# Optimization experiments

Measured on AMD Instinct MI355X. Metric: run time of the kernel, lower is better.

## Reference

```python
import jax, jax.numpy as jnp
import numpy as np

NUM_HEADS = 16
ROTARY_BASE = 10000.0


def _apply_rotary(x):
    # x: (B, S, H, D); GPT-NeoX style rotate-half over full head dim
    B, S, H, D = x.shape
    half = D // 2
    inv_freq = 1.0 / (ROTARY_BASE ** (jnp.arange(0, half, dtype=jnp.float32) / half))
    t = jnp.arange(S, dtype=jnp.float32)
    freqs = jnp.einsum('s,d->sd', t, inv_freq)          # (S, half)
    cos = jnp.cos(freqs)[None, :, None, :]               # (1, S, 1, half)
    sin = jnp.sin(freqs)[None, :, None, :]
    x1, x2 = x[..., :half], x[..., half:]
    return jnp.concatenate([x1 * cos - x2 * sin, x2 * cos + x1 * sin], axis=-1).astype(x.dtype)


def setup_inputs() -> dict:
    key = jax.random.key(0)
    k0, k1, k2 = jax.random.split(key, 3)
    B, S, E = 2, 2048, 2048
    x = jax.random.normal(k0, (B, S, E), dtype=jnp.float32)
    wqkv = jax.random.normal(k1, (3 * E, E), dtype=jnp.float32) * 0.02
    bqkv = jnp.zeros((3 * E,), dtype=jnp.float32)
    wout = jax.random.normal(k2, (E, E), dtype=jnp.float32) * 0.02
    bout = jnp.zeros((E,), dtype=jnp.float32)
    return {"x": x, "wqkv": wqkv, "bqkv": bqkv, "wout": wout, "bout": bout}


def reference(x, wqkv, bqkv, wout, bout):
    B, S, E = x.shape
    H = NUM_HEADS
    D = E // H
    # fused QKV projection: (B, S, 3, H, D)
    qkv = (jnp.einsum('bse,fe->bsf', x, wqkv) + bqkv).reshape(B, S, 3, H, D)
    q, k, v = qkv[:, :, 0], qkv[:, :, 1], qkv[:, :, 2]
    q = _apply_rotary(q)
    k = _apply_rotary(k)
    scale = 1.0 / jnp.sqrt(jnp.float32(D))
    scores = jnp.einsum('bthd,bshd->bhts', q, k) * scale  # (B, H, S, S)
    causal_mask = jnp.triu(jnp.full((S, S), -10000.0, dtype=scores.dtype), 1)
    attn = jax.nn.softmax(scores + causal_mask, axis=-1)
    ctx = jnp.einsum('bhts,bshd->bthd', attn, v).reshape(B, S, E)
    return jnp.einsum('bse,fe->bsf', ctx, wout) + bout
```

## Files before the change

kernel.cpp:

```cpp
#include <hip/hip_runtime.h>
#include <math.h>

#define BB 2
#define SS 2048
#define EE 2048
#define HH 16
#define DD 128
#define FF 6144

typedef __attribute__((ext_vector_type(8))) short short8;
typedef __attribute__((ext_vector_type(4))) float floatx4;

static __device__ __forceinline__ unsigned short f2bf(float x) {
  unsigned u = __float_as_uint(x);
  u += 0x7fffu + ((u >> 16) & 1u);
  return (unsigned short)(u >> 16);
}
static __device__ __forceinline__ float bf2f(unsigned short h) {
  return __uint_as_float((unsigned)h << 16);
}

#define GLOAD_LDS16(gp, lp)                                       \
  __builtin_amdgcn_global_load_lds(                               \
      (const __attribute__((address_space(1))) void*)(gp),        \
      (__attribute__((address_space(3))) void*)(lp), 16, 0, 0)

__global__ __launch_bounds__(256) void cast_f32_bf16(
    const float* __restrict__ in, unsigned short* __restrict__ out, int n4) {
  const int i = blockIdx.x * 256 + threadIdx.x;
  if (i >= n4) return;
  const float4 v = ((const float4*)in)[i];
  ushort4 o;
  o.x = f2bf(v.x); o.y = f2bf(v.y); o.z = f2bf(v.z); o.w = f2bf(v.w);
  ((ushort4*)out)[i] = o;
}

static __device__ __forceinline__ void store_out(float* p, float v) { *p = v; }
static __device__ __forceinline__ void store_out(unsigned short* p, float v) {
  *p = f2bf(v);
}

template <typename OutT>
__global__ __launch_bounds__(256) void gemm_bf16_mfma(
    const unsigned short* __restrict__ A, const unsigned short* __restrict__ Bt,
    const float* __restrict__ bias, OutT* __restrict__ C,
    int M, int N, int K) {
  __shared__ unsigned short As[2][128][32];
  __shared__ unsigned short Bs[2][128][32];
  const int tid = threadIdx.x;
  const int L = tid & 63;
  const int w = tid >> 6;
  const int m0 = blockIdx.y * 128;
  const int n0 = blockIdx.x * 128;

  const int i0 = w * 2;
  const int lrow = L >> 2;
  const int lcol = (L & 3) * 8;
  const size_t a_off0 = (size_t)(m0 + (i0 + 0) * 16 + lrow) * K + lcol;
  const size_t a_off1 = (size_t)(m0 + (i0 + 1) * 16 + lrow) * K + lcol;
  const size_t b_off0 = (size_t)(n0 + (i0 + 0) * 16 + lrow) * K + lcol;
  const size_t b_off1 = (size_t)(n0 + (i0 + 1) * 16 + lrow) * K + lcol;

  const int wr = (w >> 1) * 64;
  const int wc = (w & 1) * 64;
  const int lane16 = L & 15;
  const int quad = L >> 4;

  floatx4 acc[4][4] = {};

  GLOAD_LDS16(A + a_off0, &As[0][(i0 + 0) * 16][0]);
  GLOAD_LDS16(A + a_off1, &As[0][(i0 + 1) * 16][0]);
  GLOAD_LDS16(Bt + b_off0, &Bs[0][(i0 + 0) * 16][0]);
  GLOAD_LDS16(Bt + b_off1, &Bs[0][(i0 + 1) * 16][0]);

  for (int k0 = 0; k0 < K; k0 += 32) {
    const int cur = (k0 >> 5) & 1;
    __syncthreads();
    if (k0 + 32 < K) {
      const int nxt = cur ^ 1;
      GLOAD_LDS16(A + a_off0 + k0 + 32, &As[nxt][(i0 + 0) * 16][0]);
      GLOAD_LDS16(A + a_off1 + k0 + 32, &As[nxt][(i0 + 1) * 16][0]);
      GLOAD_LDS16(Bt + b_off0 + k0 + 32, &Bs[nxt][(i0 + 0) * 16][0]);
      GLOAD_LDS16(Bt + b_off1 + k0 + 32, &Bs[nxt][(i0 + 1) * 16][0]);
    }

    short8 a[4], b[4];
#pragma unroll
    for (int mi = 0; mi < 4; ++mi)
      a[mi] = *(const short8*)(&As[cur][wr + mi * 16 + lane16][quad * 8]);
#pragma unroll
    for (int ni = 0; ni < 4; ++ni)
      b[ni] = *(const short8*)(&Bs[cur][wc + ni * 16 + lane16][quad * 8]);
#pragma unroll
    for (int mi = 0; mi < 4; ++mi)
#pragma unroll
      for (int ni = 0; ni < 4; ++ni)
        acc[mi][ni] = __builtin_amdgcn_mfma_f32_16x16x32_bf16(
            a[mi], b[ni], acc[mi][ni], 0, 0, 0);
  }

#pragma unroll
  for (int ni = 0; ni < 4; ++ni) {
    const int col = n0 + wc + ni * 16 + lane16;
    const float bv = bias[col];
#pragma unroll
    for (int mi = 0; mi < 4; ++mi) {
      const int row = m0 + wr + mi * 16 + quad * 4;
#pragma unroll
      for (int r = 0; r < 4; ++r)
        store_out(&C[(size_t)(row + r) * N + col], acc[mi][ni][r] + bv);
    }
  }
}

template <typename OutT>
__global__ __launch_bounds__(512, 2) void gemm256_8ph(
    const unsigned short* __restrict__ A, const unsigned short* __restrict__ Bt,
    const float* __restrict__ bias, OutT* __restrict__ C,
    int M, int N, int K) {
  __shared__ __align__(16) unsigned short As[2][16384];
  __shared__ __align__(16) unsigned short Bs[2][16384];

  const int tid = threadIdx.x;
  const int w = tid >> 6;
  const int L = tid & 63;
  const int lane16 = L & 15;
  const int quad = L >> 4;
  const int wm = w >> 2;
  const int wn = w & 3;

  const int nby = M >> 8;
  const int q8 = gridDim.x >> 3;
  const int wg = (blockIdx.x & 7) * q8 + (blockIdx.x >> 3);
  const int by = wg % nby;
  const int bx = wg / nby;
  const int m0 = by << 8;
  const int n0 = bx << 8;

  const int lA = ((w >> 1) << 4) + (L >> 2);
  const int scol = ((w & 1) << 5) + (((L & 3) * 8) ^ ((L & 32) ? 16 : 0));
  unsigned aoff[4], boff[4];
#pragma unroll
  for (int j = 0; j < 4; ++j) {
    const int ra = ((j & 1) << 7) | ((j >> 1) << 6) | lA;
    aoff[j] = (unsigned)(m0 + ra) * (unsigned)K + scol;
    const int lB = j * 64 + lA;
    const int rB = (((lB >> 5) & 3) << 6) | (((lB >> 7) & 1) << 5) | (lB & 31);
    boff[j] = (unsigned)(n0 + rB) * (unsigned)K + scol;
  }
  const int ldst = w * 512;

  const int sq = (quad * 8) ^ ((lane16 & 8) << 1);
  const int rbase = lane16 * 32 + sq;

  floatx4 acc[8][4] = {};

  GLOAD_LDS16(A + aoff[0], &As[0][0 * 4096 + ldst]);
  GLOAD_LDS16(A + aoff[1], &As[0][1 * 4096 + ldst]);
  GLOAD_LDS16(Bt + boff[0], &Bs[0][0 * 4096 + ldst]);
  GLOAD_LDS16(Bt + boff[1], &Bs[0][1 * 4096 + ldst]);
  GLOAD_LDS16(Bt + boff[2], &Bs[0][2 * 4096 + ldst]);
  GLOAD_LDS16(Bt + boff[3], &Bs[0][3 * 4096 + ldst]);
  GLOAD_LDS16(A + aoff[2], &As[0][2 * 4096 + ldst]);
  GLOAD_LDS16(A + aoff[3], &As[0][3 * 4096 + ldst]);
  GLOAD_LDS16(A + aoff[0] + 64, &As[1][0 * 4096 + ldst]);
  GLOAD_LDS16(A + aoff[1] + 64, &As[1][1 * 4096 + ldst]);
  GLOAD_LDS16(Bt + boff[0] + 64, &Bs[1][0 * 4096 + ldst]);
  GLOAD_LDS16(Bt + boff[1] + 64, &Bs[1][1 * 4096 + ldst]);
  GLOAD_LDS16(Bt + boff[2] + 64, &Bs[1][2 * 4096 + ldst]);
  GLOAD_LDS16(Bt + boff[3] + 64, &Bs[1][3 * 4096 + ldst]);
  GLOAD_LDS16(A + aoff[2] + 64, &As[1][2 * 4096 + ldst]);
  GLOAD_LDS16(A + aoff[3] + 64, &As[1][3 * 4096 + ldst]);
  asm volatile("s_waitcnt vmcnt(8)" ::: "memory");
  __builtin_amdgcn_sched_barrier(0);
  __builtin_amdgcn_s_barrier();

  const int NT = K >> 6;
  short8 a[4][2], b0[2][2], b1[2][2];

  for (int t = 0; t < NT; ++t) {
    const int c = t & 1;
    const unsigned kn2 = (unsigned)(t + 2) << 6;
    const unsigned short* Ac = &As[c][0];
    const unsigned short* Bc = &Bs[c][0];

#pragma unroll
    for (int i = 0; i < 4; ++i)
#pragma unroll
      for (int kk = 0; kk < 2; ++kk)
        a[i][kk] = *(const short8*)(Ac + ((wm * 4 + i) * 2 + kk) * 512 + rbase);
#pragma unroll
    for (int j = 0; j < 2; ++j)
#pragma unroll
      for (int kk = 0; kk < 2; ++kk)
        b0[j][kk] = *(const short8*)(Bc + ((wn * 2 + j) * 2 + kk) * 512 + rbase);
    __builtin_amdgcn_s_setprio(1);
#pragma unroll
    for (int i = 0; i < 4; ++i)
#pragma unroll
      for (int j = 0; j < 2; ++j)
#pragma unroll
        for (int kk = 0; kk < 2; ++kk)
          acc[i][j] = __builtin_amdgcn_mfma_f32_16x16x32_bf16(
              a[i][kk], b0[j][kk], acc[i][j], 0, 0, 0);
    __builtin_amdgcn_s_setprio(0);
    __builtin_amdgcn_sched_barrier(0);
    __builtin_amdgcn_s_barrier();

#pragma unroll
    for (int j = 0; j < 2; ++j)
#pragma unroll
      for (int kk = 0; kk < 2; ++kk)
        b1[j][kk] =
            *(const short8*)(Bc + ((8 + wn * 2 + j) * 2 + kk) * 512 + rbase);
    GLOAD_LDS16(A + aoff[0] + kn2, &As[c][0 * 4096 + ldst]);
    GLOAD_LDS16(A + aoff[1] + kn2, &As[c][1 * 4096 + ldst]);
    GLOAD_LDS16(Bt + boff[0] + kn2, &Bs[c][0 * 4096 + ldst]);
    GLOAD_LDS16(Bt + boff[1] + kn2, &Bs[c][1 * 4096 + ldst]);
    __builtin_amdgcn_s_setprio(1);
#pragma unroll
    for (int i = 0; i < 4; ++i)
#pragma unroll
      for (int j = 0; j < 2; ++j)
#pragma unroll
        for (int kk = 0; kk < 2; ++kk)
          acc[i][2 + j] = __builtin_amdgcn_mfma_f32_16x16x32_bf16(
              a[i][kk], b1[j][kk], acc[i][2 + j], 0, 0, 0);
    __builtin_amdgcn_s_setprio(0);
    __builtin_amdgcn_sched_barrier(0);
    __builtin_amdgcn_s_barrier();

#pragma unroll
    for (int i = 0; i < 4; ++i)
#pragma unroll
      for (int kk = 0; kk < 2; ++kk)
        a[i][kk] =
            *(const short8*)(Ac + ((8 + wm * 4 + i) * 2 + kk) * 512 + rbase);
    GLOAD_LDS16(Bt + boff[2] + kn2, &Bs[c][2 * 4096 + ldst]);
    GLOAD_LDS16(Bt + boff[3] + kn2, &Bs[c][3 * 4096 + ldst]);
    __builtin_amdgcn_s_setprio(1);
#pragma unroll
    for (int i = 0; i < 4; ++i)
#pragma unroll
      for (int j = 0; j < 2; ++j)
#pragma unroll
        for (int kk = 0; kk < 2; ++kk)
          acc[4 + i][2 + j] = __builtin_amdgcn_mfma_f32_16x16x32_bf16(
              a[i][kk], b1[j][kk], acc[4 + i][2 + j], 0, 0, 0);
    __builtin_amdgcn_s_setprio(0);
    __builtin_amdgcn_sched_barrier(0);
    __builtin_amdgcn_s_barrier();

    GLOAD_LDS16(A + aoff[2] + kn2, &As[c][2 * 4096 + ldst]);
    GLOAD_LDS16(A + aoff[3] + kn2, &As[c][3 * 4096 + ldst]);
    __builtin_amdgcn_s_setprio(1);
#pragma unroll
    for (int i = 0; i < 4; ++i)
#pragma unroll
      for (int j = 0; j < 2; ++j)
#pragma unroll
        for (int kk = 0; kk < 2; ++kk)
          acc[4 + i][j] = __builtin_amdgcn_mfma_f32_16x16x32_bf16(
              a[i][kk], b0[j][kk], acc[4 + i][j], 0, 0, 0);
    __builtin_amdgcn_s_setprio(0);
    asm volatile("s_waitcnt vmcnt(8)" ::: "memory");
    __builtin_amdgcn_sched_barrier(0);
    __builtin_amdgcn_s_barrier();
  }

#pragma unroll
  for (int ni = 0; ni < 4; ++ni) {
    const int col = n0 + wn * 64 + ni * 16 + lane16;
    const float bv = bias[col];
#pragma unroll
    for (int mi = 0; mi < 8; ++mi) {
      const int row = m0 + wm * 128 + mi * 16 + quad * 4;
#pragma unroll
      for (int r = 0; r < 4; ++r)
        store_out(&C[(size_t)(row + r) * N + col], acc[mi][ni][r] + bv);
    }
  }
}

__global__ __launch_bounds__(256) void rotary_kernel(unsigned short* __restrict__ qkv) {
  const int idx = blockIdx.x * blockDim.x + threadIdx.x;
  const int d = idx & 63;
  const int h = (idx >> 6) & (HH - 1);
  const int s = (idx >> 10) & (SS - 1);
  const int b = idx >> 21;

  const float inv_freq = __expf(-(float)d * 0.14391156509f);
  float sn, c;
  __sincosf((float)s * inv_freq, &sn, &c);

  const size_t base = ((size_t)b * SS + s) * FF + h * DD + d;
  unsigned short* q = qkv + base;
  unsigned short* k = qkv + base + EE;

  const float q1 = bf2f(q[0]), q2 = bf2f(q[64]);
  q[0]  = f2bf(q1 * c - q2 * sn);
  q[64] = f2bf(q2 * c + q1 * sn);
  const float k1 = bf2f(k[0]), k2 = bf2f(k[64]);
  k[0]  = f2bf(k1 * c - k2 * sn);
  k[64] = f2bf(k2 * c + k1 * sn);
}

__global__ __launch_bounds__(256) void transpose_v(
    const unsigned short* __restrict__ qkv, unsigned short* __restrict__ vt) {
  __shared__ unsigned short T[64][72];
  const int t = threadIdx.x;
  const int s0 = blockIdx.x * 64;
  const int d0 = blockIdx.y * 64;
  const int bh = blockIdx.z;
  const int b = bh >> 4, h = bh & 15;
  {
    const int r = t >> 2, c = (t & 3) * 16;
    const unsigned short* src =
        qkv + ((size_t)b * SS + s0 + r) * FF + 2 * EE + h * DD + d0 + c;
    const uint4 u0 = *(const uint4*)src;
    const uint4 u1 = *(const uint4*)(src + 8);
    *(uint4*)&T[r][c] = u0;
    *(uint4*)&T[r][c + 8] = u1;
  }
  __syncthreads();
  {
    const int rr = t >> 2, cc = (t & 3) * 16;
    unsigned short vals[16];
#pragma unroll
    for (int j = 0; j < 16; ++j) vals[j] = T[cc + j][rr];
    unsigned short* dst =
        vt + (size_t)bh * DD * SS + (size_t)(d0 + rr) * SS + s0 + cc;
    *(uint4*)dst = *(uint4*)&vals[0];
    *(uint4*)(dst + 8) = *(uint4*)&vals[8];
  }
}

#define ATQ 128
#define ATK 32
#define SPAD 40
#define NQT (SS / ATQ)

__global__ __launch_bounds__(256, 2) void attn_mfma(
    const unsigned short* __restrict__ qkv,
    const unsigned short* __restrict__ vt,
    unsigned short* __restrict__ ctx) {
  __shared__ __align__(16) unsigned short Ksh[2][ATK * DD];
  __shared__ __align__(16) unsigned short Vsh[2][DD * ATK];
  __shared__ __align__(16) unsigned short Ssh[ATQ][SPAD];

  const int tid = threadIdx.x;
  const int L = tid & 63;
  const int w = tid >> 6;
  const int lane16 = L & 15;
  const int quad = L >> 4;

  const int flat = blockIdx.x;
  const int pi = flat >> 5;
  const int bh_lin = flat & 31;
  const int b = bh_lin >> 4;
  const int h = bh_lin & 15;
  const int bh = b * HH + h;
  const float scale = 0.08838834764831845f;

  size_t koff[2], voff[2];
  int kdst[2], vdst[2];
#pragma unroll
  for (int j = 0; j < 2; ++j) {
    const int ck = j * 256 + tid;
    const int kk = ck >> 4;
    const int cgk = (ck & 15) ^ (kk & 15);
    koff[j] = ((size_t)b * SS + kk) * FF + EE + h * DD + cgk * 8;
    kdst[j] = (j * 256 + w * 64) * 8;
    const int d = ck >> 2;
    const int cgv = (ck & 3) ^ (d & 3);
    voff[j] = (size_t)bh * DD * SS + (size_t)d * SS + cgv * 8;
    vdst[j] = kdst[j];
  }

#pragma unroll 1
  for (int phase = 0; phase < 2; ++phase) {
    const int qb = phase ? pi : (NQT - 1 - pi);
    const int q0 = qb * ATQ;

    short8 qf[2][4];
#pragma unroll
    for (int mi = 0; mi < 2; ++mi) {
      const int q = q0 + w * 32 + mi * 16 + lane16;
      const unsigned short* qp =
          qkv + ((size_t)b * SS + q) * FF + h * DD + quad * 8;
#pragma unroll
      for (int dc = 0; dc < 4; ++dc)
        qf[mi][dc] = *(const short8*)(qp + dc * 32);
    }

    floatx4 acc[8][2] = {};
    float m_i[2] = {-3.0e38f, -3.0e38f};
    float l_i[2] = {0.0f, 0.0f};

    const int nkt = 4 * qb + 4;
    const int mykt = 4 * qb + w;

#pragma unroll
    for (int j = 0; j < 2; ++j) {
      GLOAD_LDS16(qkv + koff[j], &Ksh[0][kdst[j]]);
      GLOAD_LDS16(vt + voff[j], &Vsh[0][vdst[j]]);
    }

    for (int kt = 0; kt < nkt; ++kt) {
      const int cur = kt & 1;
      __syncthreads();
      if (kt + 1 < nkt) {
        const size_t ka = (size_t)(kt + 1) * ATK * FF;
        const int va = (kt + 1) * ATK;
#pragma unroll
        for (int j = 0; j < 2; ++j) {
          GLOAD_LDS16(qkv + koff[j] + ka, &Ksh[cur ^ 1][kdst[j]]);
          GLOAD_LDS16(vt + voff[j] + va, &Vsh[cur ^ 1][vdst[j]]);
        }
      }
      if (kt > mykt) continue;
      const int k0 = kt * ATK;
      const unsigned short* Kc = Ksh[cur];
      const unsigned short* Vc = Vsh[cur];

      floatx4 st[2][2] = {};
#pragma unroll
      for (int kkt = 0; kkt < 2; ++kkt) {
        const unsigned short* krow = Kc + (kkt * 16 + lane16) * 128;
#pragma unroll
        for (int dc = 0; dc < 4; ++dc) {
          const short8 kf =
              *(const short8*)(krow + ((dc * 4 + quad) ^ lane16) * 8);
#pragma unroll
          for (int mi = 0; mi < 2; ++mi)
            st[kkt][mi] = __builtin_amdgcn_mfma_f32_16x16x32_bf16(
                kf, qf[mi][dc], st[kkt][mi], 0, 0, 0);
        }
      }

      const bool needmask = (kt == mykt);
#pragma unroll
      for (int mi = 0; mi < 2; ++mi) {
        const int q_glob = q0 + w * 32 + mi * 16 + lane16;
#pragma unroll
        for (int kkt = 0; kkt < 2; ++kkt) {
          const int kkb = k0 + kkt * 16 + quad * 4;
#pragma unroll
          for (int r = 0; r < 4; ++r) {
            float v = st[kkt][mi][r] * scale;
            if (needmask && (kkb + r) > q_glob) v = -3.0e38f;
            st[kkt][mi][r] = v;
          }
        }
      }

      float alpha[2];
#pragma unroll
      for (int mi = 0; mi < 2; ++mi) {
        float tm = -3.0e38f;
#pragma unroll
        for (int kkt = 0; kkt < 2; ++kkt)
#pragma unroll
          for (int r = 0; r < 4; ++r) tm = fmaxf(tm, st[kkt][mi][r]);
        tm = fmaxf(tm, __shfl_xor(tm, 16));
        tm = fmaxf(tm, __shfl_xor(tm, 32));
        const float mn = fmaxf(m_i[mi], tm);
        alpha[mi] = __expf(m_i[mi] - mn);
        m_i[mi] = mn;

        float rs = 0.0f;
#pragma unroll
        for (int kkt = 0; kkt < 2; ++kkt)
#pragma unroll
          for (int r = 0; r < 4; ++r) {
            const float p = __expf(st[kkt][mi][r] - mn);
            st[kkt][mi][r] = p;
            rs += p;
          }
        rs += __shfl_xor(rs, 16);
        rs += __shfl_xor(rs, 32);
        l_i[mi] = l_i[mi] * alpha[mi] + rs;

#pragma unroll
        for (int kkt = 0; kkt < 2; ++kkt) {
          ushort4 pk;
          pk.x = f2bf(st[kkt][mi][0]);
          pk.y = f2bf(st[kkt][mi][1]);
          pk.z = f2bf(st[kkt][mi][2]);
          pk.w = f2bf(st[kkt][mi][3]);
          *(ushort4*)(&Ssh[w * 32 + mi * 16 + lane16][kkt * 16 + quad * 4]) =
              pk;
        }
      }

#pragma unroll
      for (int dt = 0; dt < 8; ++dt)
#pragma unroll
        for (int mi = 0; mi < 2; ++mi)
#pragma unroll
          for (int r = 0; r < 4; ++r) acc[dt][mi][r] *= alpha[mi];

      short8 pa[2];
#pragma unroll
      for (int mi = 0; mi < 2; ++mi)
        pa[mi] = *(const short8*)(&Ssh[w * 32 + mi * 16 + lane16][quad * 8]);
      const int vpos = (quad ^ (lane16 & 3)) * 8;
#pragma unroll
      for (int dt = 0; dt < 8; ++dt) {
        const short8 vf =
            *(const short8*)(Vc + (dt * 16 + lane16) * 32 + vpos);
#pragma unroll
        for (int mi = 0; mi < 2; ++mi)
          acc[dt][mi] = __builtin_amdgcn_mfma_f32_16x16x32_bf16(
              vf, pa[mi], acc[dt][mi], 0, 0, 0);
      }
    }

#pragma unroll
    for (int mi = 0; mi < 2; ++mi) {
      const float inv = 1.0f / l_i[mi];
      const int q = q0 + w * 32 + mi * 16 + lane16;
      unsigned short* op = ctx + ((size_t)b * SS + q) * EE + h * DD + quad * 4;
#pragma unroll
      for (int dt = 0; dt < 8; ++dt) {
        ushort4 o;
        o.x = f2bf(acc[dt][mi][0] * inv);
        o.y = f2bf(acc[dt][mi][1] * inv);
        o.z = f2bf(acc[dt][mi][2] * inv);
        o.w = f2bf(acc[dt][mi][3] * inv);
        *(ushort4*)(op + dt * 16) = o;
      }
    }
  }
}

extern "C" void kernel_launch(void* const* d_in, const int* in_sizes, int n_in,
                              void* d_out, int out_size, void* d_ws,
                              size_t ws_size, hipStream_t stream) {
  const float* x    = (const float*)d_in[0];
  const float* wqkv = (const float*)d_in[1];
  const float* bqkv = (const float*)d_in[2];
  const float* wout = (const float*)d_in[3];
  const float* bout = (const float*)d_in[4];
  float* out = (float*)d_out;

  unsigned short* qkvb = (unsigned short*)d_ws;
  unsigned short* xb   = qkvb + (size_t)25165824;
  unsigned short* wqb  = xb + (size_t)8388608;
  unsigned short* ctxb = wqb + (size_t)12582912;
  unsigned short* wob  = ctxb + (size_t)8388608;
  unsigned short* vtb  = wob + (size_t)4194304;

  const int M = BB * SS;

  cast_f32_bf16<<<8192, 256, 0, stream>>>(x, xb, 2097152);
  cast_f32_bf16<<<12288, 256, 0, stream>>>(wqkv, wqb, 3145728);
  cast_f32_bf16<<<4096, 256, 0, stream>>>(wout, wob, 1048576);

  {
    gemm256_8ph<unsigned short><<<dim3(384), 512, 0, stream>>>(
        xb, wqb, bqkv, qkvb, M, FF, EE);
  }
  {
    const int total = BB * SS * HH * 64;
    rotary_kernel<<<total / 256, 256, 0, stream>>>(qkvb);
  }
  {
    dim3 grid(SS / 64, DD / 64, BB * HH);
    transpose_v<<<grid, 256, 0, stream>>>(qkvb, vtb);
  }
  {
    attn_mfma<<<dim3(256), 256, 0, stream>>>(qkvb, vtb, ctxb);
  }
  {
    dim3 grid(EE / 128, M / 128);
    gemm_bf16_mfma<float><<<grid, 256, 0, stream>>>(
        ctxb, wob, bout, out, M, EE, EE);
  }
}
```

Baseline: 438.2 us.

## Retile QKV GEMM to 256x192 blocks with two-phase pipeline

The QKV projection GEMM moves from 256x256 tiles with a four-phase schedule to 256x192 tiles, giving 512 blocks instead of 384. This spreads work more evenly across the GPU's compute units. The main loop now has two phases per k-step, with A prefetched one step ahead into the other buffer and B prefetched two steps ahead into the current buffer. Each block reuses less data per tile, and the new prefetch and wait scheme changes how load latency is hidden.

```diff
diff --git a/kernel.cpp b/kernel.cpp
--- a/kernel.cpp
+++ b/kernel.cpp
@@ -114,12 +114,12 @@
 }
 
 template <typename OutT>
-__global__ __launch_bounds__(512, 2) void gemm256_8ph(
+__global__ __launch_bounds__(512, 2) void gemm_bf16_256x192(
     const unsigned short* __restrict__ A, const unsigned short* __restrict__ Bt,
     const float* __restrict__ bias, OutT* __restrict__ C,
     int M, int N, int K) {
   __shared__ __align__(16) unsigned short As[2][16384];
-  __shared__ __align__(16) unsigned short Bs[2][16384];
+  __shared__ __align__(16) unsigned short Bs[2][12288];
 
   const int tid = threadIdx.x;
   const int w = tid >> 6;
@@ -135,142 +135,106 @@
   const int by = wg % nby;
   const int bx = wg / nby;
   const int m0 = by << 8;
-  const int n0 = bx << 8;
+  const int n0 = bx * 192;
 
   const int lA = ((w >> 1) << 4) + (L >> 2);
   const int scol = ((w & 1) << 5) + (((L & 3) * 8) ^ ((L & 32) ? 16 : 0));
-  unsigned aoff[4], boff[4];
-#pragma unroll
-  for (int j = 0; j < 4; ++j) {
-    const int ra = ((j & 1) << 7) | ((j >> 1) << 6) | lA;
-    aoff[j] = (unsigned)(m0 + ra) * (unsigned)K + scol;
-    const int lB = j * 64 + lA;
-    const int rB = (((lB >> 5) & 3) << 6) | (((lB >> 7) & 1) << 5) | (lB & 31);
-    boff[j] = (unsigned)(n0 + rB) * (unsigned)K + scol;
-  }
+  unsigned aoff[4], boff[3];
+#pragma unroll
+  for (int j = 0; j < 4; ++j)
+    aoff[j] = (unsigned)(m0 + j * 64 + lA) * (unsigned)K + scol;
+#pragma unroll
+  for (int j = 0; j < 3; ++j)
+    boff[j] = (unsigned)(n0 + j * 64 + lA) * (unsigned)K + scol;
   const int ldst = w * 512;
 
   const int sq = (quad * 8) ^ ((lane16 & 8) << 1);
   const int rbase = lane16 * 32 + sq;
 
-  floatx4 acc[8][4] = {};
+  floatx4 acc[8][3] = {};
 
   GLOAD_LDS16(A + aoff[0], &As[0][0 * 4096 + ldst]);
   GLOAD_LDS16(A + aoff[1], &As[0][1 * 4096 + ldst]);
+  GLOAD_LDS16(A + aoff[2], &As[0][2 * 4096 + ldst]);
+  GLOAD_LDS16(A + aoff[3], &As[0][3 * 4096 + ldst]);
   GLOAD_LDS16(Bt + boff[0], &Bs[0][0 * 4096 + ldst]);
   GLOAD_LDS16(Bt + boff[1], &Bs[0][1 * 4096 + ldst]);
   GLOAD_LDS16(Bt + boff[2], &Bs[0][2 * 4096 + ldst]);
-  GLOAD_LDS16(Bt + boff[3], &Bs[0][3 * 4096 + ldst]);
-  GLOAD_LDS16(A + aoff[2], &As[0][2 * 4096 + ldst]);
-  GLOAD_LDS16(A + aoff[3], &As[0][3 * 4096 + ldst]);
-  GLOAD_LDS16(A + aoff[0] + 64, &As[1][0 * 4096 + ldst]);
-  GLOAD_LDS16(A + aoff[1] + 64, &As[1][1 * 4096 + ldst]);
   GLOAD_LDS16(Bt + boff[0] + 64, &Bs[1][0 * 4096 + ldst]);
   GLOAD_LDS16(Bt + boff[1] + 64, &Bs[1][1 * 4096 + ldst]);
   GLOAD_LDS16(Bt + boff[2] + 64, &Bs[1][2 * 4096 + ldst]);
-  GLOAD_LDS16(Bt + boff[3] + 64, &Bs[1][3 * 4096 + ldst]);
-  GLOAD_LDS16(A + aoff[2] + 64, &As[1][2 * 4096 + ldst]);
-  GLOAD_LDS16(A + aoff[3] + 64, &As[1][3 * 4096 + ldst]);
-  asm volatile("s_waitcnt vmcnt(8)" ::: "memory");
+  asm volatile("s_waitcnt vmcnt(3)" ::: "memory");
   __builtin_amdgcn_sched_barrier(0);
   __builtin_amdgcn_s_barrier();
 
   const int NT = K >> 6;
-  short8 a[4][2], b0[2][2], b1[2][2];
+  short8 a[4][2], b[3][2];
 
   for (int t = 0; t < NT; ++t) {
     const int c = t & 1;
+    const unsigned kn1 = (unsigned)(t + 1) << 6;
     const unsigned kn2 = (unsigned)(t + 2) << 6;
     const unsigned short* Ac = &As[c][0];
     const unsigned short* Bc = &Bs[c][0];
 
 #pragma unroll
-    for (int i = 0; i < 4; ++i)
+    for (int mi = 0; mi < 4; ++mi)
 #pragma unroll
       for (int kk = 0; kk < 2; ++kk)
-        a[i][kk] = *(const short8*)(Ac + ((wm * 4 + i) * 2 + kk) * 512 + rbase);
-#pragma unroll
-    for (int j = 0; j < 2; ++j)
+        a[mi][kk] = *(const short8*)(Ac + (wm * 2) * 4096 +
+                                     ((mi * 2 + kk) * 512) + rbase);
+#pragma unroll
+    for (int ni = 0; ni < 3; ++ni) {
+      const int f = wn * 3 + ni;
 #pragma unroll
       for (int kk = 0; kk < 2; ++kk)
-        b0[j][kk] = *(const short8*)(Bc + ((wn * 2 + j) * 2 + kk) * 512 + rbase);
+        b[ni][kk] = *(const short8*)(Bc + (f >> 2) * 4096 +
+                                     (((f & 3) * 2 + kk) * 512) + rbase);
+    }
+    GLOAD_LDS16(A + aoff[0] + kn1, &As[c ^ 1][0 * 4096 + ldst]);
+    GLOAD_LDS16(A + aoff[1] + kn1, &As[c ^ 1][1 * 4096 + ldst]);
+    GLOAD_LDS16(A + aoff[2] + kn1, &As[c ^ 1][2 * 4096 + ldst]);
+    GLOAD_LDS16(A + aoff[3] + kn1, &As[c ^ 1][3 * 4096 + ldst]);
     __builtin_amdgcn_s_setprio(1);
 #pragma unroll
-    for (int i = 0; i < 4; ++i)
-#pragma unroll
-      for (int j = 0; j < 2; ++j)
+    for (int mi = 0; mi < 4; ++mi)
+#pragma unroll
+      for (int ni = 0; ni < 3; ++ni)
 #pragma unroll
         for (int kk = 0; kk < 2; ++kk)
-          acc[i][j] = __builtin_amdgcn_mfma_f32_16x16x32_bf16(
-              a[i][kk], b0[j][kk], acc[i][j], 0, 0, 0);
+          acc[mi][ni] = __builtin_amdgcn_mfma_f32_16x16x32_bf16(
+              a[mi][kk], b[ni][kk], acc[mi][ni], 0, 0, 0);
     __builtin_amdgcn_s_setprio(0);
     __builtin_amdgcn_sched_barrier(0);
     __builtin_amdgcn_s_barrier();
 
 #pragma unroll
-    for (int j = 0; j < 2; ++j)
+    for (int mi = 0; mi < 4; ++mi)
 #pragma unroll
       for (int kk = 0; kk < 2; ++kk)
-        b1[j][kk] =
-            *(const short8*)(Bc + ((8 + wn * 2 + j) * 2 + kk) * 512 + rbase);
-    GLOAD_LDS16(A + aoff[0] + kn2, &As[c][0 * 4096 + ldst]);
-    GLOAD_LDS16(A + aoff[1] + kn2, &As[c][1 * 4096 + ldst]);
+        a[mi][kk] = *(const short8*)(Ac + (wm * 2 + 1) * 4096 +
+                                     ((mi * 2 + kk) * 512) + rbase);
     GLOAD_LDS16(Bt + boff[0] + kn2, &Bs[c][0 * 4096 + ldst]);
     GLOAD_LDS16(Bt + boff[1] + kn2, &Bs[c][1 * 4096 + ldst]);
+    GLOAD_LDS16(Bt + boff[2] + kn2, &Bs[c][2 * 4096 + ldst]);
     __builtin_amdgcn_s_setprio(1);
 #pragma unroll
-    for (int i = 0; i < 4; ++i)
-#pragma unroll
-      for (int j = 0; j < 2; ++j)
+    for (int mi = 0; mi < 4; ++mi)
+#pragma unroll
+      for (int ni = 0; ni < 3; ++ni)
 #pragma unroll
         for (int kk = 0; kk < 2; ++kk)
-          acc[i][2 + j] = __builtin_amdgcn_mfma_f32_16x16x32_bf16(
-              a[i][kk], b1[j][kk], acc[i][2 + j], 0, 0, 0);
+          acc[4 + mi][ni] = __builtin_amdgcn_mfma_f32_16x16x32_bf16(
+              a[mi][kk], b[ni][kk], acc[4 + mi][ni], 0, 0, 0);
     __builtin_amdgcn_s_setprio(0);
+    asm volatile("s_waitcnt vmcnt(3)" ::: "memory");
     __builtin_amdgcn_sched_barrier(0);
     __builtin_amdgcn_s_barrier();
-
-#pragma unroll
-    for (int i = 0; i < 4; ++i)
-#pragma unroll
-      for (int kk = 0; kk < 2; ++kk)
-        a[i][kk] =
-            *(const short8*)(Ac + ((8 + wm * 4 + i) * 2 + kk) * 512 + rbase);
-    GLOAD_LDS16(Bt + boff[2] + kn2, &Bs[c][2 * 4096 + ldst]);
-    GLOAD_LDS16(Bt + boff[3] + kn2, &Bs[c][3 * 4096 + ldst]);
-    __builtin_amdgcn_s_setprio(1);
-#pragma unroll
-    for (int i = 0; i < 4; ++i)
-#pragma unroll
-      for (int j = 0; j < 2; ++j)
-#pragma unroll
-        for (int kk = 0; kk < 2; ++kk)
-          acc[4 + i][2 + j] = __builtin_amdgcn_mfma_f32_16x16x32_bf16(
-              a[i][kk], b1[j][kk], acc[4 + i][2 + j], 0, 0, 0);
-    __builtin_amdgcn_s_setprio(0);
-    __builtin_amdgcn_sched_barrier(0);
-    __builtin_amdgcn_s_barrier();
-
-    GLOAD_LDS16(A + aoff[2] + kn2, &As[c][2 * 4096 + ldst]);
-    GLOAD_LDS16(A + aoff[3] + kn2, &As[c][3 * 4096 + ldst]);
-    __builtin_amdgcn_s_setprio(1);
-#pragma unroll
-    for (int i = 0; i < 4; ++i)
-#pragma unroll
-      for (int j = 0; j < 2; ++j)
-#pragma unroll
-        for (int kk = 0; kk < 2; ++kk)
-          acc[4 + i][j] = __builtin_amdgcn_mfma_f32_16x16x32_bf16(
-              a[i][kk], b0[j][kk], acc[4 + i][j], 0, 0, 0);
-    __builtin_amdgcn_s_setprio(0);
-    asm volatile("s_waitcnt vmcnt(8)" ::: "memory");
-    __builtin_amdgcn_sched_barrier(0);
-    __builtin_amdgcn_s_barrier();
-  }
-
-#pragma unroll
-  for (int ni = 0; ni < 4; ++ni) {
-    const int col = n0 + wn * 64 + ni * 16 + lane16;
+  }
+
+#pragma unroll
+  for (int ni = 0; ni < 3; ++ni) {
+    const int col = n0 + wn * 48 + ni * 16 + lane16;
     const float bv = bias[col];
 #pragma unroll
     for (int mi = 0; mi < 8; ++mi) {
@@ -558,7 +522,7 @@
   cast_f32_bf16<<<4096, 256, 0, stream>>>(wout, wob, 1048576);
 
   {
-    gemm256_8ph<unsigned short><<<dim3(384), 512, 0, stream>>>(
+    gemm_bf16_256x192<unsigned short><<<dim3(512), 512, 0, stream>>>(
         xb, wqb, bqkv, qkvb, M, FF, EE);
   }
   {
```

Result: faster. 415.6 us (-5.2%).
